# Kernel optimization log

Measured on AMD Instinct MI355X. Metric: run time of the kernel, lower is better.

Reference implementation:

```python
import jax, jax.numpy as jnp
import numpy as np

N = 100000   # nodes
E = 1600000  # edges
F = 64       # node_features


def setup_inputs() -> dict:
    key = jax.random.key(0)
    ks = jax.random.split(key, 8)
    x = jax.random.normal(ks[0], (N, F), dtype=jnp.float32)
    edge_index = jax.random.randint(ks[1], (2, E), 0, N, dtype=jnp.int64)
    edge_weight = jax.random.uniform(ks[2], (E,), dtype=jnp.float32)
    # degrees consistent with the graph (in-degree + 1 to avoid zeros)
    deg = jax.ops.segment_sum(jnp.ones((E,), jnp.float32), edge_index[1], num_segments=N) + 1.0
    W_init = jax.random.normal(ks[3], (F, F), dtype=jnp.float32) / np.sqrt(F)
    gru_wih = jax.random.normal(ks[4], (3 * F, F), dtype=jnp.float32) / np.sqrt(F)
    gru_whh = jax.random.normal(ks[5], (3 * F, F), dtype=jnp.float32) / np.sqrt(F)
    gru_bih = jnp.zeros((3 * F,), jnp.float32)
    gru_bhh = jnp.zeros((3 * F,), jnp.float32)
    lin_w = jax.random.normal(ks[6], (1, F), dtype=jnp.float32) / np.sqrt(F)
    lin_b = jnp.zeros((1,), jnp.float32)
    return {
        "x": x, "edge_index": edge_index, "edge_weight": edge_weight,
        "deg": deg, "target_num": N, "W_init": W_init,
        "gru_wih": gru_wih, "gru_whh": gru_whh,
        "gru_bih": gru_bih, "gru_bhh": gru_bhh,
        "lin_w": lin_w, "lin_b": lin_b,
    }


def _evolve_weight(W, wih, whh, bih, bhh):
    # EvolveGCN-O: GRU with the [F,F] weight matrix as both input and hidden.
    # Rows of W are the "batch"; PyTorch GRU gate order: r, z, n.
    gx = W @ wih.T + bih   # [F, 3F]
    gh = W @ whh.T + bhh   # [F, 3F]
    gx_r, gx_z, gx_n = jnp.split(gx, 3, axis=-1)
    gh_r, gh_z, gh_n = jnp.split(gh, 3, axis=-1)
    r = jax.nn.sigmoid(gx_r + gh_r)
    z = jax.nn.sigmoid(gx_z + gh_z)
    n = jnp.tanh(gx_n + r * gh_n)
    return (1.0 - z) * n + z * W


def reference(x, edge_index, edge_weight, deg, target_num, W_init,
              gru_wih, gru_whh, gru_bih, gru_bhh, lin_w, lin_b):
    # 1) evolve GCN weight with GRU
    W = _evolve_weight(W_init, gru_wih, gru_whh, gru_bih, gru_bhh)
    # 2) GCN conv with fixed evolved W: sym-normalized gather-scatter
    src, dst = edge_index[0], edge_index[1]
    dinv = jax.lax.rsqrt(deg)                       # [N]
    norm = edge_weight * dinv[src] * dinv[dst]      # [E]
    xw = x @ W                                      # [N, F]
    msgs = norm[:, None] * xw[src]                  # [E, F] (irregular gather)
    h = jax.ops.segment_sum(msgs, dst, num_segments=x.shape[0])  # scatter-add
    # 3) keep target nodes, ReLU, linear projection to 1
    h = jax.nn.relu(h[:target_num])
    out = h @ lin_w.T + lin_b                       # [target_num, 1]
    return out
```

## Files before the change

### kernel.cpp

```cpp
#include <hip/hip_runtime.h>
#include <hip/hip_bf16.h>

#define F 64
#define RB 128
#define RBSH 7
#define NBMAX 800
#define CHUNKA 4096
#define CAPR  2816
#define CAPR2 3200

typedef int            nt_int4   __attribute__((ext_vector_type(4)));
typedef float          nt_float4 __attribute__((ext_vector_type(4)));

__device__ __forceinline__ unsigned short f2bf(float f) {
    unsigned int u = __float_as_uint(f);
    unsigned int r = (u + 0x7FFFu + ((u >> 16) & 1u)) >> 16;
    return (unsigned short)r;
}
__device__ __forceinline__ unsigned int pack2bf(float lo, float hi) {
    return (unsigned int)f2bf(lo) | ((unsigned int)f2bf(hi) << 16);
}

__global__ void evolve_kernel(const float* __restrict__ W,
                              const float* __restrict__ wih,
                              const float* __restrict__ whh,
                              const float* __restrict__ bih,
                              const float* __restrict__ bhh,
                              float* __restrict__ wt) {
    int t = blockIdx.x * blockDim.x + threadIdx.x;
    if (t >= F * F) return;
    int i = t >> 6;
    int j = t & 63;
    const float* Wi = W + i * F;
    float gxr = bih[j], gxz = bih[F + j], gxn = bih[2 * F + j];
    float ghr = bhh[j], ghz = bhh[F + j], ghn = bhh[2 * F + j];
#pragma unroll
    for (int k = 0; k < F; ++k) {
        float wv = Wi[k];
        gxr += wv * wih[(j) * F + k];
        gxz += wv * wih[(F + j) * F + k];
        gxn += wv * wih[(2 * F + j) * F + k];
        ghr += wv * whh[(j) * F + k];
        ghz += wv * whh[(F + j) * F + k];
        ghn += wv * whh[(2 * F + j) * F + k];
    }
    float r = 1.0f / (1.0f + expf(-(gxr + ghr)));
    float z = 1.0f / (1.0f + expf(-(gxz + ghz)));
    float n = tanhf(gxn + r * ghn);
    float wnew = (1.0f - z) * n + z * Wi[j];
    wt[j * F + i] = wnew;
}

__global__ void init_gcur_kernel(int* __restrict__ gcur, int NB) {
    int t = threadIdx.x;
    if (t < NB) gcur[t] = t * CAPR;
}

__global__ void __launch_bounds__(256, 1) xw_kernel(
        const float* __restrict__ x,
        const float* __restrict__ wt,
        const float* __restrict__ deg,
        unsigned short* __restrict__ xw16, int N) {
    int i = blockIdx.x;
    int rowblk  = (i >> 5) * 8 + (i & 7);
    int quarter = (i >> 3) & 3;
    int r = rowblk * 256 + threadIdx.x;
    if (r >= N) return;
    float xr[F];
    const nt_float4* xp = (const nt_float4*)(x + (size_t)r * F);
#pragma unroll
    for (int q = 0; q < F / 4; ++q) {
        nt_float4 v = xp[q];
        xr[4 * q + 0] = v.x; xr[4 * q + 1] = v.y;
        xr[4 * q + 2] = v.z; xr[4 * q + 3] = v.w;
    }
    float dinv = rsqrtf(deg[r]);
    const float* wbase = wt + quarter * 16 * F;
    unsigned int o[8];
#pragma unroll
    for (int cb = 0; cb < 4; ++cb) {
        const float* w0 = wbase + (4 * cb) * F;
        float a0 = 0.f, a1 = 0.f, a2 = 0.f, a3 = 0.f;
#pragma unroll
        for (int k = 0; k < F; ++k) {
            float xv = xr[k];
            a0 += xv * w0[k];
            a1 += xv * w0[F + k];
            a2 += xv * w0[2 * F + k];
            a3 += xv * w0[3 * F + k];
        }
        o[2 * cb]     = pack2bf(a0 * dinv, a1 * dinv);
        o[2 * cb + 1] = pack2bf(a2 * dinv, a3 * dinv);
    }
    nt_int4* dst = (nt_int4*)(xw16 + (size_t)r * F + quarter * 16);
#pragma unroll
    for (int q = 0; q < 2; ++q) {
        nt_int4 v;
        v.x = (int)o[4 * q + 0]; v.y = (int)o[4 * q + 1];
        v.z = (int)o[4 * q + 2]; v.w = (int)o[4 * q + 3];
        dst[q] = v;
    }
}

__global__ void __launch_bounds__(1024) passA_kernel(
        const int* __restrict__ ei, const float* __restrict__ ew,
        int* __restrict__ gcur,
        unsigned long long* __restrict__ rec, int E, int NB) {
    __shared__ int lh[NBMAX];
    __shared__ int lcur[NBMAX];
    int t = threadIdx.x;
    for (int i = t; i < NB; i += 1024) lh[i] = 0;
    __syncthreads();
    int base = blockIdx.x * CHUNKA;
#pragma unroll
    for (int it = 0; it < CHUNKA / 1024; ++it) {
        int e = base + it * 1024 + t;
        if (e < E) atomicAdd(&lh[ei[E + e] >> RBSH], 1);
    }
    __syncthreads();
    for (int i = t; i < NB; i += 1024) {
        int c = lh[i];
        lcur[i] = c ? atomicAdd(&gcur[i], c) : 0;
    }
    __syncthreads();
#pragma unroll
    for (int it = 0; it < CHUNKA / 1024; ++it) {
        int e = base + it * 1024 + t;
        if (e < E) {
            int dst = ei[E + e];
            int src = ei[e];
            float w = ew[e];
            unsigned int q = (unsigned int)(w * 32767.0f + 0.5f);
            int b = dst >> RBSH;
            int p = atomicAdd(&lcur[b], 1);
            unsigned long long r = ((unsigned long long)(dst & (RB - 1)) << 32)
                                 | ((unsigned long long)((unsigned int)src) << 15) | q;
            rec[p] = r;
        }
    }
}

__global__ void sortB_kernel(const unsigned long long* __restrict__ rec,
                             const int* __restrict__ gcur,
                             unsigned int* __restrict__ rec2,
                             int2* __restrict__ node_off2,
                             int N, int NB) {
    __shared__ int cnt[RB];
    __shared__ int pex[RB];
    __shared__ int cur[RB];
    int b = blockIdx.x;
    int t = threadIdx.x;
    int beg = b * CAPR;
    int end = gcur[b];
    int beg2 = b * CAPR2;
    if (t < RB) cnt[t] = 0;
    __syncthreads();
    for (int i = beg + t; i < end; i += 256)
        atomicAdd(&cnt[(int)(rec[i] >> 32)], 1);
    __syncthreads();
    if (t < RB) pex[t] = (cnt[t] + 3) & ~3;
    __syncthreads();
    for (int o = 1; o < RB; o <<= 1) {
        int v = (t < RB && t >= o) ? pex[t - o] : 0;
        __syncthreads();
        if (t < RB) pex[t] += v;
        __syncthreads();
    }
    int node0 = b << RBSH;
    if (t < RB) {
        int pcnt = (cnt[t] + 3) & ~3;
        int excl = pex[t] - pcnt;
        pex[t] = excl;
        cur[t] = excl;
        int node = node0 + t;
        if (node < N) node_off2[node] = make_int2(beg2 + excl, cnt[t]);
    }
    __syncthreads();
    for (int i = beg + t; i < end; i += 256) {
        unsigned long long r = rec[i];
        int dl = (int)(r >> 32);
        int p = atomicAdd(&cur[dl], 1);
        rec2[beg2 + p] = (unsigned int)r;
    }
    __syncthreads();
    if (t < RB) {
        int c = cnt[t];
        int pcnt = (c + 3) & ~3;
        int base2 = beg2 + pex[t];
        for (int k = c; k < pcnt; ++k) rec2[base2 + k] = 0;
    }
}

__global__ void segsum_kernel(const unsigned short* __restrict__ xw16,
                              const int2* __restrict__ node_off2,
                              const unsigned int* __restrict__ rec2,
                              const float* __restrict__ deg,
                              const float* __restrict__ lw,
                              const float* __restrict__ lb,
                              float* __restrict__ out, int M) {
    int gid = blockIdx.x * blockDim.x + threadIdx.x;
    int node = gid >> 6;
    int lane = threadIdx.x & 63;
    if (node >= M) return;
    int2 nf = node_off2[node];
    int beg = nf.x;
    int iters = (nf.y + 3) >> 2;
    int eg = lane >> 4;
    int fq = lane & 15;
    unsigned int flo = (unsigned int)(fq << 3);
    float a0 = 0.f, a1 = 0.f, a2 = 0.f, a3 = 0.f;
    const char* xb = (const char*)xw16;
    const unsigned int* rp = rec2 + beg + eg;
#pragma unroll 4
    for (int i = 0; i < iters; ++i) {
        unsigned int r = rp[4 * i];
        unsigned int off = ((r >> 8) & 0xFFFFFF80u) + flo;
        uint2 u = *(const uint2*)(xb + off);
        float q = (float)(r & 32767u);
        a0 += q * __uint_as_float(u.x << 16);
        a1 += q * __uint_as_float(u.x & 0xFFFF0000u);
        a2 += q * __uint_as_float(u.y << 16);
        a3 += q * __uint_as_float(u.y & 0xFFFF0000u);
    }
    a0 += __shfl_xor(a0, 16, 64); a0 += __shfl_xor(a0, 32, 64);
    a1 += __shfl_xor(a1, 16, 64); a1 += __shfl_xor(a1, 32, 64);
    a2 += __shfl_xor(a2, 16, 64); a2 += __shfl_xor(a2, 32, 64);
    a3 += __shfl_xor(a3, 16, 64); a3 += __shfl_xor(a3, 32, 64);
    float s = fmaxf(a0, 0.f) * lw[4 * fq + 0]
            + fmaxf(a1, 0.f) * lw[4 * fq + 1]
            + fmaxf(a2, 0.f) * lw[4 * fq + 2]
            + fmaxf(a3, 0.f) * lw[4 * fq + 3];
#pragma unroll
    for (int o = 8; o; o >>= 1) s += __shfl_xor(s, o, 64);
    if (lane == 0)
        out[node] = s * ((1.0f / 32767.0f) * rsqrtf(deg[node])) + lb[0];
}

extern "C" void kernel_launch(void* const* d_in, const int* in_sizes, int n_in,
                              void* d_out, int out_size, void* d_ws, size_t ws_size,
                              hipStream_t stream) {
    const float* x   = (const float*)d_in[0];
    const int*   ei  = (const int*)d_in[1];
    const float* ew  = (const float*)d_in[2];
    const float* deg = (const float*)d_in[3];
    const float* W0  = (const float*)d_in[5];
    const float* wih = (const float*)d_in[6];
    const float* whh = (const float*)d_in[7];
    const float* bih = (const float*)d_in[8];
    const float* bhh = (const float*)d_in[9];
    const float* lw  = (const float*)d_in[10];
    const float* lb  = (const float*)d_in[11];
    float* out = (float*)d_out;

    int N = in_sizes[0] / F;
    int E = in_sizes[1] / 2;
    int M = out_size;
    int NB = (N + RB - 1) / RB;

    float*              wt        = (float*)d_ws;
    unsigned short*     xw16      = (unsigned short*)(wt + 8192);
    unsigned long long* rec       = (unsigned long long*)(xw16 + (size_t)N * F);
    unsigned int*       rec2      = (unsigned int*)(rec + (size_t)NB * CAPR);
    int2*               node_off2 = (int2*)(rec2 + (size_t)NB * CAPR2);
    int*                gcur      = (int*)(node_off2 + N + 4);

    evolve_kernel<<<(F * F + 255) / 256, 256, 0, stream>>>(W0, wih, whh, bih, bhh, wt);

    init_gcur_kernel<<<1, 1024, 0, stream>>>(gcur, NB);

    {
        int nrb8 = (((N + 255) / 256) + 7) & ~7;
        xw_kernel<<<4 * nrb8, 256, 0, stream>>>(x, wt, deg, xw16, N);
    }

    passA_kernel<<<(E + CHUNKA - 1) / CHUNKA, 1024, 0, stream>>>(ei, ew, gcur, rec, E, NB);

    sortB_kernel<<<NB, 256, 0, stream>>>(rec, gcur, rec2, node_off2, N, NB);

    {
        long long threads = (long long)M * 64;
        int blocks = (int)((threads + 255) / 256);
        segsum_kernel<<<blocks, 256, 0, stream>>>(xw16, node_off2, rec2, deg, lw, lb, out, M);
    }
}
```

Measured before the change: 143.3 us.

## Fuse gcur init, cache edge loads in passA, two nodes per wave in segsum

```diff
diff --git a/kernel.cpp b/kernel.cpp
--- a/kernel.cpp
+++ b/kernel.cpp
@@ -51,16 +51,16 @@
     wt[j * F + i] = wnew;
 }
 
-__global__ void init_gcur_kernel(int* __restrict__ gcur, int NB) {
-    int t = threadIdx.x;
-    if (t < NB) gcur[t] = t * CAPR;
-}
-
 __global__ void __launch_bounds__(256, 1) xw_kernel(
         const float* __restrict__ x,
         const float* __restrict__ wt,
         const float* __restrict__ deg,
-        unsigned short* __restrict__ xw16, int N) {
+        unsigned short* __restrict__ xw16,
+        int* __restrict__ gcur, int N, int NB) {
+    if (blockIdx.x < 4) {
+        int gi = blockIdx.x * 256 + threadIdx.x;
+        if (gi < NB) gcur[gi] = gi * CAPR;
+    }
     int i = blockIdx.x;
     int rowblk  = (i >> 5) * 8 + (i & 7);
     int quarter = (i >> 3) & 3;
@@ -112,10 +112,19 @@
     for (int i = t; i < NB; i += 1024) lh[i] = 0;
     __syncthreads();
     int base = blockIdx.x * CHUNKA;
+    int  dstR[4], srcR[4];
+    float ewR[4];
+    bool ok[4];
 #pragma unroll
     for (int it = 0; it < CHUNKA / 1024; ++it) {
         int e = base + it * 1024 + t;
-        if (e < E) atomicAdd(&lh[ei[E + e] >> RBSH], 1);
+        ok[it] = (e < E);
+        if (ok[it]) {
+            dstR[it] = ei[E + e];
+            srcR[it] = ei[e];
+            ewR[it]  = ew[e];
+            atomicAdd(&lh[dstR[it] >> RBSH], 1);
+        }
     }
     __syncthreads();
     for (int i = t; i < NB; i += 1024) {
@@ -125,26 +134,23 @@
     __syncthreads();
 #pragma unroll
     for (int it = 0; it < CHUNKA / 1024; ++it) {
-        int e = base + it * 1024 + t;
-        if (e < E) {
-            int dst = ei[E + e];
-            int src = ei[e];
-            float w = ew[e];
-            unsigned int q = (unsigned int)(w * 32767.0f + 0.5f);
-            int b = dst >> RBSH;
+        if (ok[it]) {
+            unsigned int q = (unsigned int)(ewR[it] * 32767.0f + 0.5f);
+            int b = dstR[it] >> RBSH;
             int p = atomicAdd(&lcur[b], 1);
-            unsigned long long r = ((unsigned long long)(dst & (RB - 1)) << 32)
-                                 | ((unsigned long long)((unsigned int)src) << 15) | q;
+            unsigned long long r = ((unsigned long long)(dstR[it] & (RB - 1)) << 32)
+                                 | ((unsigned long long)((unsigned int)srcR[it]) << 15) | q;
             rec[p] = r;
         }
     }
 }
 
-__global__ void sortB_kernel(const unsigned long long* __restrict__ rec,
-                             const int* __restrict__ gcur,
-                             unsigned int* __restrict__ rec2,
-                             int2* __restrict__ node_off2,
-                             int N, int NB) {
+__global__ void __launch_bounds__(512) sortB_kernel(
+        const unsigned long long* __restrict__ rec,
+        const int* __restrict__ gcur,
+        unsigned int* __restrict__ rec2,
+        int2* __restrict__ node_off2,
+        int N, int NB) {
     __shared__ int cnt[RB];
     __shared__ int pex[RB];
     __shared__ int cur[RB];
@@ -155,7 +161,7 @@
     int beg2 = b * CAPR2;
     if (t < RB) cnt[t] = 0;
     __syncthreads();
-    for (int i = beg + t; i < end; i += 256)
+    for (int i = beg + t; i < end; i += 512)
         atomicAdd(&cnt[(int)(rec[i] >> 32)], 1);
     __syncthreads();
     if (t < RB) pex[t] = (cnt[t] + 3) & ~3;
@@ -176,7 +182,7 @@
         if (node < N) node_off2[node] = make_int2(beg2 + excl, cnt[t]);
     }
     __syncthreads();
-    for (int i = beg + t; i < end; i += 256) {
+    for (int i = beg + t; i < end; i += 512) {
         unsigned long long r = rec[i];
         int dl = (int)(r >> 32);
         int p = atomicAdd(&cur[dl], 1);
@@ -199,21 +205,32 @@
                               const float* __restrict__ lb,
                               float* __restrict__ out, int M) {
     int gid = blockIdx.x * blockDim.x + threadIdx.x;
-    int node = gid >> 6;
+    int wid = gid >> 6;
     int lane = threadIdx.x & 63;
-    if (node >= M) return;
-    int2 nf = node_off2[node];
-    int beg = nf.x;
-    int iters = (nf.y + 3) >> 2;
+    int node0 = wid * 2;
+    if (node0 >= M) return;
+    int node1 = node0 + 1;
+    bool has1 = (node1 < M);
+    int2 nf0 = node_off2[node0];
+    int2 nf1 = has1 ? node_off2[node1] : make_int2(0, 0);
     int eg = lane >> 4;
     int fq = lane & 15;
     unsigned int flo = (unsigned int)(fq << 3);
+    const char* xb = (const char*)xw16;
+    const unsigned int* rp0 = rec2 + nf0.x + eg;
+    const unsigned int* rp1 = rec2 + nf1.x + eg;
+    int it0 = (nf0.y + 3) >> 2;
+    int it1 = has1 ? ((nf1.y + 3) >> 2) : 0;
+    float lw0 = lw[4 * fq + 0], lw1 = lw[4 * fq + 1];
+    float lw2 = lw[4 * fq + 2], lw3 = lw[4 * fq + 3];
+    const float esc = 1.0f / 32767.0f;
+
+    unsigned int r1f = (it1 > 0) ? rp1[0] : 0u;
+
     float a0 = 0.f, a1 = 0.f, a2 = 0.f, a3 = 0.f;
-    const char* xb = (const char*)xw16;
-    const unsigned int* rp = rec2 + beg + eg;
 #pragma unroll 4
-    for (int i = 0; i < iters; ++i) {
-        unsigned int r = rp[4 * i];
+    for (int i = 0; i < it0; ++i) {
+        unsigned int r = rp0[4 * i];
         unsigned int off = ((r >> 8) & 0xFFFFFF80u) + flo;
         uint2 u = *(const uint2*)(xb + off);
         float q = (float)(r & 32767u);
@@ -222,18 +239,51 @@
         a2 += q * __uint_as_float(u.y << 16);
         a3 += q * __uint_as_float(u.y & 0xFFFF0000u);
     }
+
+    uint2 u1f = make_uint2(0u, 0u);
+    if (it1 > 0)
+        u1f = *(const uint2*)(xb + (((r1f >> 8) & 0xFFFFFF80u) + flo));
+
     a0 += __shfl_xor(a0, 16, 64); a0 += __shfl_xor(a0, 32, 64);
     a1 += __shfl_xor(a1, 16, 64); a1 += __shfl_xor(a1, 32, 64);
     a2 += __shfl_xor(a2, 16, 64); a2 += __shfl_xor(a2, 32, 64);
     a3 += __shfl_xor(a3, 16, 64); a3 += __shfl_xor(a3, 32, 64);
-    float s = fmaxf(a0, 0.f) * lw[4 * fq + 0]
-            + fmaxf(a1, 0.f) * lw[4 * fq + 1]
-            + fmaxf(a2, 0.f) * lw[4 * fq + 2]
-            + fmaxf(a3, 0.f) * lw[4 * fq + 3];
-#pragma unroll
-    for (int o = 8; o; o >>= 1) s += __shfl_xor(s, o, 64);
-    if (lane == 0)
-        out[node] = s * ((1.0f / 32767.0f) * rsqrtf(deg[node])) + lb[0];
+    float s0 = fmaxf(a0, 0.f) * lw0 + fmaxf(a1, 0.f) * lw1
+             + fmaxf(a2, 0.f) * lw2 + fmaxf(a3, 0.f) * lw3;
+#pragma unroll
+    for (int o = 8; o; o >>= 1) s0 += __shfl_xor(s0, o, 64);
+    if (lane == 0) out[node0] = s0 * (esc * rsqrtf(deg[node0])) + lb[0];
+
+    if (!has1) return;
+
+    float b0 = 0.f, b1 = 0.f, b2 = 0.f, b3 = 0.f;
+    if (it1 > 0) {
+        float q = (float)(r1f & 32767u);
+        b0 += q * __uint_as_float(u1f.x << 16);
+        b1 += q * __uint_as_float(u1f.x & 0xFFFF0000u);
+        b2 += q * __uint_as_float(u1f.y << 16);
+        b3 += q * __uint_as_float(u1f.y & 0xFFFF0000u);
+    }
+#pragma unroll 4
+    for (int i = 1; i < it1; ++i) {
+        unsigned int r = rp1[4 * i];
+        unsigned int off = ((r >> 8) & 0xFFFFFF80u) + flo;
+        uint2 u = *(const uint2*)(xb + off);
+        float q = (float)(r & 32767u);
+        b0 += q * __uint_as_float(u.x << 16);
+        b1 += q * __uint_as_float(u.x & 0xFFFF0000u);
+        b2 += q * __uint_as_float(u.y << 16);
+        b3 += q * __uint_as_float(u.y & 0xFFFF0000u);
+    }
+    b0 += __shfl_xor(b0, 16, 64); b0 += __shfl_xor(b0, 32, 64);
+    b1 += __shfl_xor(b1, 16, 64); b1 += __shfl_xor(b1, 32, 64);
+    b2 += __shfl_xor(b2, 16, 64); b2 += __shfl_xor(b2, 32, 64);
+    b3 += __shfl_xor(b3, 16, 64); b3 += __shfl_xor(b3, 32, 64);
+    float s1 = fmaxf(b0, 0.f) * lw0 + fmaxf(b1, 0.f) * lw1
+             + fmaxf(b2, 0.f) * lw2 + fmaxf(b3, 0.f) * lw3;
+#pragma unroll
+    for (int o = 8; o; o >>= 1) s1 += __shfl_xor(s1, o, 64);
+    if (lane == 0) out[node1] = s1 * (esc * rsqrtf(deg[node1])) + lb[0];
 }
 
 extern "C" void kernel_launch(void* const* d_in, const int* in_sizes, int n_in,
@@ -266,19 +316,17 @@
 
     evolve_kernel<<<(F * F + 255) / 256, 256, 0, stream>>>(W0, wih, whh, bih, bhh, wt);
 
-    init_gcur_kernel<<<1, 1024, 0, stream>>>(gcur, NB);
-
     {
         int nrb8 = (((N + 255) / 256) + 7) & ~7;
-        xw_kernel<<<4 * nrb8, 256, 0, stream>>>(x, wt, deg, xw16, N);
+        xw_kernel<<<4 * nrb8, 256, 0, stream>>>(x, wt, deg, xw16, gcur, N, NB);
     }
 
     passA_kernel<<<(E + CHUNKA - 1) / CHUNKA, 1024, 0, stream>>>(ei, ew, gcur, rec, E, NB);
 
-    sortB_kernel<<<NB, 256, 0, stream>>>(rec, gcur, rec2, node_off2, N, NB);
+    sortB_kernel<<<NB, 512, 0, stream>>>(rec, gcur, rec2, node_off2, N, NB);
 
     {
-        long long threads = (long long)M * 64;
+        long long threads = (long long)((M + 1) / 2) * 64;
         int blocks = (int)((threads + 255) / 256);
         segsum_kernel<<<blocks, 256, 0, stream>>>(xw16, node_off2, rec2, deg, lw, lb, out, M);
     }
```

After: 137.0 us. 4.4% less time.
